# Kernel optimization log

Measured on AMD Instinct MI355X. Metric: run time of the kernel, lower is better.

## Reference

```python
import jax, jax.numpy as jnp
import numpy as np

B, BLOCK_NUM, BLOCK_LEN, DIM = 4, 32, 128, 1024
HEADS = 16
DH = DIM // HEADS  # 64
SEQ_LEN = BLOCK_NUM * BLOCK_LEN  # 4096
LN_EPS = 1e-3  # keras LayerNormalization default epsilon
NEG = -1e10


def setup_inputs() -> dict:
    key = jax.random.key(0)
    ks = jax.random.split(key, 6)
    s = 1.0 / np.sqrt(DIM)
    return {
        "inputs": jax.random.normal(ks[0], (B, BLOCK_NUM, BLOCK_LEN, DIM), jnp.float32),
        "mask": jax.random.randint(ks[1], (B, SEQ_LEN, DIM), 0, 2, jnp.int32),
        "w1": jax.random.normal(ks[2], (DIM, DIM), jnp.float32) * s,
        "b1": jnp.zeros((DIM,), jnp.float32),
        "w2": jax.random.normal(ks[3], (DIM, DIM), jnp.float32) * s,
        "b2": jnp.zeros((DIM,), jnp.float32),
        "w3": jax.random.normal(ks[4], (DIM, DIM), jnp.float32) * s,
        "b3": jnp.zeros((DIM,), jnp.float32),
        "gamma": jnp.ones((DIM,), jnp.float32),
        "beta": jnp.zeros((DIM,), jnp.float32),
    }


def _split_heads(x):
    # [B, bn, bl, DIM] -> [H, B, bn, bl, DH]  (tf.split axis=-1 + concat axis=0)
    return jnp.moveaxis(x.reshape(B, BLOCK_NUM, BLOCK_LEN, HEADS, DH), 3, 0)


def reference(inputs, mask, w1, b1, w2, b2, w3, b3, gamma, beta):
    Q = _split_heads(inputs @ w1 + b1)
    K = _split_heads(inputs @ w2 + b2)
    V = _split_heads(inputs @ w3 + b3)

    # block-local attention scores: [H, B, bn, bl, bl]
    scores = jnp.einsum("hbnqd,hbnkd->hbnqk", Q, K) / np.sqrt(DH)

    # mask: [B, seq, DIM] -> [B, bn, bl, DIM] -> heads -> [H, B, bn, bl, DH]
    m = jnp.moveaxis(
        mask.astype(jnp.float32).reshape(B, BLOCK_NUM, BLOCK_LEN, HEADS, DH), 3, 0
    )
    # block_len (128) > DH (64): take first feature, tile across key axis
    m = jnp.broadcast_to(m[..., :1], (HEADS, B, BLOCK_NUM, BLOCK_LEN, BLOCK_LEN))
    scores = scores + (1.0 - m) * NEG

    attn = jax.nn.softmax(scores, axis=-1)
    out = jnp.einsum("hbnqk,hbnkd->hbnqd", attn, V)
    # merge heads: [H, B, bn, bl, DH] -> [B, bn, bl, DIM]
    out = jnp.moveaxis(out, 0, 3).reshape(B, BLOCK_NUM, BLOCK_LEN, DIM)

    res = out + inputs
    mu = res.mean(axis=-1, keepdims=True)
    var = res.var(axis=-1, keepdims=True)
    return gamma * (res - mu) * jax.lax.rsqrt(var + LN_EPS) + beta
```

## Files before the change

kernel.cpp:

```cpp
#include <hip/hip_runtime.h>
#include <hip/hip_bf16.h>
#include <stdint.h>

#define DIM 1024
#define NTOK 16384
#define SEQ 4096
#define BLKLEN 128
#define NHEAD 16
#define DH 64

typedef short bf16x8 __attribute__((ext_vector_type(8)));
typedef float f32x4 __attribute__((ext_vector_type(4)));

static __device__ __forceinline__ unsigned short f2bf(float f) {
  union { float f; uint32_t u; } v; v.f = f;
  return (unsigned short)((v.u + 0x7FFFu + ((v.u >> 16) & 1u)) >> 16);
}
static __device__ __forceinline__ float bf2f(unsigned short h) {
  union { uint32_t u; float f; } v; v.u = ((uint32_t)h) << 16;
  return v.f;
}
static __device__ __forceinline__ uint32_t pk2(float a, float b) {
  __hip_bfloat162 h = __float22bfloat162_rn(make_float2(a, b));
  union { __hip_bfloat162 h; uint32_t u; } c; c.h = h; return c.u;
}
static __device__ __forceinline__ void cvt8(float4 x, float4 y, uint4& hi, uint4& lo) {
  float f[8] = {x.x, x.y, x.z, x.w, y.x, y.y, y.z, y.w};
  uint32_t h[4], l[4];
#pragma unroll
  for (int i = 0; i < 4; ++i) {
    h[i] = pk2(f[2 * i], f[2 * i + 1]);
    union { uint32_t u; float g; } e0, e1;
    e0.u = h[i] << 16;
    e1.u = h[i] & 0xFFFF0000u;
    l[i] = pk2(f[2 * i] - e0.g, f[2 * i + 1] - e1.g);
  }
  hi = make_uint4(h[0], h[1], h[2], h[3]);
  lo = make_uint4(l[0], l[1], l[2], l[3]);
}

__global__ void wsplit_kernel(const float* __restrict__ w1, const float* __restrict__ w2,
                              const float* __restrict__ w3,
                              unsigned short* __restrict__ hi, unsigned short* __restrict__ lo) {
  const float* w = (blockIdx.z == 0) ? w1 : (blockIdx.z == 1) ? w2 : w3;
  unsigned short* hp = hi + (size_t)blockIdx.z * DIM * DIM;
  unsigned short* lp = lo + (size_t)blockIdx.z * DIM * DIM;
  __shared__ float t[64][65];
  int m0 = blockIdx.x * 64, k0 = blockIdx.y * 64;
  int tx = threadIdx.x, ty = threadIdx.y;
  for (int i = ty; i < 64; i += 4)
    t[i][tx] = w[(size_t)(k0 + i) * DIM + m0 + tx];
  __syncthreads();
  for (int i = ty; i < 64; i += 4) {
    float x = t[tx][i];
    unsigned short h = f2bf(x);
    size_t o = (size_t)(m0 + i) * DIM + k0 + tx;
    hp[o] = h;
    lp[o] = f2bf(x - bf2f(h));
  }
}

#define BK 32
#define AST 40

__global__ __launch_bounds__(256, 2) void qkv_gemm_kernel(
    const float* __restrict__ X,
    const unsigned short* __restrict__ Whi, const unsigned short* __restrict__ Wlo,
    const float* __restrict__ b1, const float* __restrict__ b2, const float* __restrict__ b3,
    float* __restrict__ Qp, float* __restrict__ Kp, float* __restrict__ Vp) {
  __shared__ unsigned short Ah[128 * AST], Al[128 * AST], Bh[128 * AST], Bl[128 * AST];

  int tile_n = blockIdx.x;
  int tile_m = blockIdx.y;
  int wsel = tile_n >> 3;
  int colw0 = (tile_n & 7) * 128;
  const unsigned short* wh = Whi + (size_t)wsel * DIM * DIM;
  const unsigned short* wl = Wlo + (size_t)wsel * DIM * DIM;
  const float* bias = (wsel == 0) ? b1 : (wsel == 1) ? b2 : b3;
  float* o = (wsel == 0) ? Qp : (wsel == 1) ? Kp : Vp;

  int t = threadIdx.x;
  int wid = t >> 6, lane = t & 63;
  int wr = wid >> 1, wc = wid & 1;

  f32x4 acc[4][4];
#pragma unroll
  for (int i = 0; i < 4; ++i)
#pragma unroll
    for (int j = 0; j < 4; ++j) acc[i][j] = (f32x4){0.f, 0.f, 0.f, 0.f};

  int srow = t >> 2;
  int kc = (t & 3) * 8;
  const size_t arow = (size_t)tile_m * 128;

  const float* pa0 = X + (arow + srow) * DIM + kc;
  const float* pa1 = X + (arow + srow + 64) * DIM + kc;
  const unsigned short* pb0 = wh + (size_t)(colw0 + srow) * DIM + kc;
  const unsigned short* pb1 = wh + (size_t)(colw0 + srow + 64) * DIM + kc;
  const unsigned short* plb0 = wl + (size_t)(colw0 + srow) * DIM + kc;
  const unsigned short* plb1 = wl + (size_t)(colw0 + srow + 64) * DIM + kc;

  uint32_t lw0 = srow * AST + kc;
  uint32_t lw1 = (srow + 64) * AST + kc;

  int frow = lane & 15;
  int fk = (lane >> 4) * 8;

  float4 ra00 = *(const float4*)(pa0), ra01 = *(const float4*)(pa0 + 4);
  float4 ra10 = *(const float4*)(pa1), ra11 = *(const float4*)(pa1 + 4);
  uint4 rbh0 = *(const uint4*)(pb0), rbh1 = *(const uint4*)(pb1);
  uint4 rbl0 = *(const uint4*)(plb0), rbl1 = *(const uint4*)(plb1);

  for (int k0 = 0; k0 < DIM; k0 += BK) {
    uint4 ah0, al0, ah1, al1;
    cvt8(ra00, ra01, ah0, al0);
    cvt8(ra10, ra11, ah1, al1);
    __syncthreads();
    *(uint4*)&Ah[lw0] = ah0; *(uint4*)&Ah[lw1] = ah1;
    *(uint4*)&Al[lw0] = al0; *(uint4*)&Al[lw1] = al1;
    *(uint4*)&Bh[lw0] = rbh0; *(uint4*)&Bh[lw1] = rbh1;
    *(uint4*)&Bl[lw0] = rbl0; *(uint4*)&Bl[lw1] = rbl1;
    __syncthreads();
    if (k0 + BK < DIM) {
      int off = k0 + BK;
      ra00 = *(const float4*)(pa0 + off); ra01 = *(const float4*)(pa0 + off + 4);
      ra10 = *(const float4*)(pa1 + off); ra11 = *(const float4*)(pa1 + off + 4);
      rbh0 = *(const uint4*)(pb0 + off); rbh1 = *(const uint4*)(pb1 + off);
      rbl0 = *(const uint4*)(plb0 + off); rbl1 = *(const uint4*)(plb1 + off);
    }
    bf16x8 fah[4], fal[4], fbh[4], fbl[4];
#pragma unroll
    for (int m = 0; m < 4; ++m) {
      int r = wr * 64 + m * 16 + frow;
      fah[m] = *(const bf16x8*)&Ah[r * AST + fk];
      fal[m] = *(const bf16x8*)&Al[r * AST + fk];
    }
#pragma unroll
    for (int n = 0; n < 4; ++n) {
      int c = wc * 64 + n * 16 + frow;
      fbh[n] = *(const bf16x8*)&Bh[c * AST + fk];
      fbl[n] = *(const bf16x8*)&Bl[c * AST + fk];
    }
#pragma unroll
    for (int m = 0; m < 4; ++m)
#pragma unroll
      for (int n = 0; n < 4; ++n) {
        acc[m][n] = __builtin_amdgcn_mfma_f32_16x16x32_bf16(fah[m], fbh[n], acc[m][n], 0, 0, 0);
        acc[m][n] = __builtin_amdgcn_mfma_f32_16x16x32_bf16(fah[m], fbl[n], acc[m][n], 0, 0, 0);
        acc[m][n] = __builtin_amdgcn_mfma_f32_16x16x32_bf16(fal[m], fbh[n], acc[m][n], 0, 0, 0);
      }
  }

  int fgrp = lane >> 4;
#pragma unroll
  for (int n = 0; n < 4; ++n) {
    int col = colw0 + wc * 64 + n * 16 + frow;
    float bv = bias[col];
#pragma unroll
    for (int m = 0; m < 4; ++m) {
      size_t row = arow + wr * 64 + m * 16 + fgrp * 4;
#pragma unroll
      for (int r = 0; r < 4; ++r)
        o[(row + r) * DIM + col] = acc[m][n][r] + bv;
    }
  }
}

__global__ __launch_bounds__(256) void attn_kernel(
    const float* __restrict__ Qg, const float* __restrict__ Kg, const float* Vg,
    const int* __restrict__ mask, const float* __restrict__ inputs, float* out) {
  __shared__ float smem[128 * 132 + 128 * 68];
  float* Qt = smem;
  float* Kt = smem + 64 * 132;
  float* Pt = smem;
  float* Vs = smem + 128 * 132;

  int blk = blockIdx.x;
  int n = blk & 31;
  int b = (blk >> 5) & 3;
  int h = blk >> 7;
  size_t tok0 = (size_t)b * SEQ + (size_t)n * BLKLEN;
  int col0 = h * DH;

  int t = threadIdx.x;
  {
    int r = t >> 1;
    int d0 = (t & 1) * 32;
    const float* qp = Qg + (tok0 + r) * DIM + col0 + d0;
    const float* kp = Kg + (tok0 + r) * DIM + col0 + d0;
    const float* vp = Vg + (tok0 + r) * DIM + col0 + d0;
#pragma unroll
    for (int i = 0; i < 8; ++i) {
      float4 q4 = *(const float4*)(qp + i * 4);
      float4 k4 = *(const float4*)(kp + i * 4);
      float4 v4 = *(const float4*)(vp + i * 4);
      int d = d0 + i * 4;
      Qt[(d + 0) * 132 + r] = q4.x; Qt[(d + 1) * 132 + r] = q4.y;
      Qt[(d + 2) * 132 + r] = q4.z; Qt[(d + 3) * 132 + r] = q4.w;
      Kt[(d + 0) * 132 + r] = k4.x; Kt[(d + 1) * 132 + r] = k4.y;
      Kt[(d + 2) * 132 + r] = k4.z; Kt[(d + 3) * 132 + r] = k4.w;
      *(float4*)&Vs[r * 68 + d] = v4;
    }
  }
  __syncthreads();

  int qt = t >> 4, kt = t & 15;
  int q0 = qt * 8, k0 = kt * 8;
  float s[8][8];
#pragma unroll
  for (int i = 0; i < 8; ++i)
#pragma unroll
    for (int j = 0; j < 8; ++j) s[i][j] = 0.f;

#pragma unroll 4
  for (int d = 0; d < 64; ++d) {
    float4 qa = *(const float4*)&Qt[d * 132 + q0];
    float4 qb = *(const float4*)&Qt[d * 132 + q0 + 4];
    float4 ka = *(const float4*)&Kt[d * 132 + k0];
    float4 kb = *(const float4*)&Kt[d * 132 + k0 + 4];
    float qv[8] = {qa.x, qa.y, qa.z, qa.w, qb.x, qb.y, qb.z, qb.w};
    float kv[8] = {ka.x, ka.y, ka.z, ka.w, kb.x, kb.y, kb.z, kb.w};
#pragma unroll
    for (int i = 0; i < 8; ++i)
#pragma unroll
      for (int j = 0; j < 8; ++j) s[i][j] += qv[i] * kv[j];
  }

  float pen[8];
#pragma unroll
  for (int i = 0; i < 8; ++i)
    pen[i] = (1.0f - (float)mask[(tok0 + q0 + i) * DIM + col0]) * -1e10f;

  float mx[8], sm[8], inv[8];
#pragma unroll
  for (int i = 0; i < 8; ++i) {
    float m0 = -3.4e38f;
#pragma unroll
    for (int j = 0; j < 8; ++j) {
      s[i][j] = s[i][j] * 0.125f + pen[i];
      m0 = fmaxf(m0, s[i][j]);
    }
    mx[i] = m0;
  }
#pragma unroll
  for (int x = 1; x < 16; x <<= 1)
#pragma unroll
    for (int i = 0; i < 8; ++i) mx[i] = fmaxf(mx[i], __shfl_xor(mx[i], x));
#pragma unroll
  for (int i = 0; i < 8; ++i) {
    float a = 0.f;
#pragma unroll
    for (int j = 0; j < 8; ++j) {
      s[i][j] = __expf(s[i][j] - mx[i]);
      a += s[i][j];
    }
    sm[i] = a;
  }
#pragma unroll
  for (int x = 1; x < 16; x <<= 1)
#pragma unroll
    for (int i = 0; i < 8; ++i) sm[i] += __shfl_xor(sm[i], x);
#pragma unroll
  for (int i = 0; i < 8; ++i) inv[i] = 1.0f / sm[i];

  __syncthreads();
#pragma unroll
  for (int j = 0; j < 8; ++j)
#pragma unroll
    for (int i = 0; i < 8; ++i)
      Pt[(k0 + j) * 132 + (q0 + i)] = s[i][j] * inv[i];
  __syncthreads();

  int dt = t & 15;
  int q0b = (t >> 4) * 8;
  int dv0 = dt * 4;
  float o0[8], o1[8], o2[8], o3[8];
#pragma unroll
  for (int i = 0; i < 8; ++i) { o0[i] = 0.f; o1[i] = 0.f; o2[i] = 0.f; o3[i] = 0.f; }

#pragma unroll 4
  for (int k = 0; k < 128; ++k) {
    float4 pa = *(const float4*)&Pt[k * 132 + q0b];
    float4 pb = *(const float4*)&Pt[k * 132 + q0b + 4];
    float4 vv = *(const float4*)&Vs[k * 68 + dv0];
    float pv[8] = {pa.x, pa.y, pa.z, pa.w, pb.x, pb.y, pb.z, pb.w};
#pragma unroll
    for (int i = 0; i < 8; ++i) {
      o0[i] += pv[i] * vv.x;
      o1[i] += pv[i] * vv.y;
      o2[i] += pv[i] * vv.z;
      o3[i] += pv[i] * vv.w;
    }
  }
#pragma unroll
  for (int i = 0; i < 8; ++i) {
    size_t idx = (tok0 + q0b + i) * DIM + col0 + dv0;
    float4 inp = *(const float4*)(inputs + idx);
    float4 r;
    r.x = o0[i] + inp.x; r.y = o1[i] + inp.y; r.z = o2[i] + inp.z; r.w = o3[i] + inp.w;
    *(float4*)(out + idx) = r;
  }
}

__global__ __launch_bounds__(256) void ln_kernel(float* __restrict__ io,
                                                 const float* __restrict__ gamma,
                                                 const float* __restrict__ beta) {
  int row = blockIdx.x;
  int t = threadIdx.x;
  float4 x = *(const float4*)(io + (size_t)row * DIM + t * 4);
  float s = x.x + x.y + x.z + x.w;
  float q = x.x * x.x + x.y * x.y + x.z * x.z + x.w * x.w;
#pragma unroll
  for (int off = 1; off < 64; off <<= 1) {
    s += __shfl_xor(s, off);
    q += __shfl_xor(q, off);
  }
  __shared__ float red[8];
  int wid = t >> 6, lane = t & 63;
  if (lane == 0) { red[wid] = s; red[wid + 4] = q; }
  __syncthreads();
  s = red[0] + red[1] + red[2] + red[3];
  q = red[4] + red[5] + red[6] + red[7];
  float mu = s * (1.0f / 1024.0f);
  float var = q * (1.0f / 1024.0f) - mu * mu;
  float rs = 1.0f / sqrtf(var + 1e-3f);
  float4 g = *(const float4*)(gamma + t * 4);
  float4 be = *(const float4*)(beta + t * 4);
  float4 r;
  r.x = g.x * (x.x - mu) * rs + be.x;
  r.y = g.y * (x.y - mu) * rs + be.y;
  r.z = g.z * (x.z - mu) * rs + be.z;
  r.w = g.w * (x.w - mu) * rs + be.w;
  *(float4*)(io + (size_t)row * DIM + t * 4) = r;
}

extern "C" void kernel_launch(void* const* d_in, const int* in_sizes, int n_in,
                              void* d_out, int out_size, void* d_ws, size_t ws_size,
                              hipStream_t stream) {
  (void)in_sizes; (void)n_in; (void)out_size; (void)ws_size;
  const float* inputs = (const float*)d_in[0];
  const int* mask = (const int*)d_in[1];
  const float* w1 = (const float*)d_in[2];
  const float* b1 = (const float*)d_in[3];
  const float* w2 = (const float*)d_in[4];
  const float* b2 = (const float*)d_in[5];
  const float* w3 = (const float*)d_in[6];
  const float* b3 = (const float*)d_in[7];
  const float* gamma = (const float*)d_in[8];
  const float* beta = (const float*)d_in[9];
  float* out = (float*)d_out;

  char* ws = (char*)d_ws;
  unsigned short* Whi = (unsigned short*)(ws);
  unsigned short* Wlo = (unsigned short*)(ws + ((size_t)6 << 20));
  float* Q = (float*)(ws + ((size_t)12 << 20));
  float* K = (float*)(ws + ((size_t)76 << 20));
  float* V = out;

  hipLaunchKernelGGL(wsplit_kernel, dim3(16, 16, 3), dim3(64, 4), 0, stream,
                     w1, w2, w3, Whi, Wlo);
  hipLaunchKernelGGL(qkv_gemm_kernel, dim3(24, 128), dim3(256), 0, stream,
                     inputs, Whi, Wlo, b1, b2, b3, Q, K, V);
  hipLaunchKernelGGL(attn_kernel, dim3(2048), dim3(256), 0, stream,
                     Q, K, V, mask, inputs, out);
  hipLaunchKernelGGL(ln_kernel, dim3(NTOK), dim3(256), 0, stream,
                     out, gamma, beta);
}
```

Measured before the change: 658.6 us.

## Drop activation low-part in QKV GEMM and store attention Q/K/P as bf16

The QKV GEMM stops splitting the input activations into hi/lo bf16 parts, which removes one of three MFMAs per tile and the Al shared buffer, and raises the occupancy hint to 4. The attention kernel now stores Q, K and the probability matrix in shared memory as bf16 instead of fp32, which halves LDS traffic and footprint and allows two blocks per CU. Both changes lower numerical precision and could push the output past the accuracy tolerance.

```diff
diff --git a/kernel.cpp b/kernel.cpp
--- a/kernel.cpp
+++ b/kernel.cpp
@@ -24,19 +24,13 @@
   __hip_bfloat162 h = __float22bfloat162_rn(make_float2(a, b));
   union { __hip_bfloat162 h; uint32_t u; } c; c.h = h; return c.u;
 }
-static __device__ __forceinline__ void cvt8(float4 x, float4 y, uint4& hi, uint4& lo) {
-  float f[8] = {x.x, x.y, x.z, x.w, y.x, y.y, y.z, y.w};
-  uint32_t h[4], l[4];
-#pragma unroll
-  for (int i = 0; i < 4; ++i) {
-    h[i] = pk2(f[2 * i], f[2 * i + 1]);
-    union { uint32_t u; float g; } e0, e1;
-    e0.u = h[i] << 16;
-    e1.u = h[i] & 0xFFFF0000u;
-    l[i] = pk2(f[2 * i] - e0.g, f[2 * i + 1] - e1.g);
-  }
-  hi = make_uint4(h[0], h[1], h[2], h[3]);
-  lo = make_uint4(l[0], l[1], l[2], l[3]);
+static __device__ __forceinline__ void up2(uint32_t w, float& a, float& b) {
+  union { uint32_t u; float f; } x, y;
+  x.u = w << 16; y.u = w & 0xFFFF0000u;
+  a = x.f; b = y.f;
+}
+static __device__ __forceinline__ uint4 cvt4(float4 x, float4 y) {
+  return make_uint4(pk2(x.x, x.y), pk2(x.z, x.w), pk2(y.x, y.y), pk2(y.z, y.w));
 }
 
 __global__ void wsplit_kernel(const float* __restrict__ w1, const float* __restrict__ w2,
@@ -63,12 +57,12 @@
 #define BK 32
 #define AST 40
 
-__global__ __launch_bounds__(256, 2) void qkv_gemm_kernel(
+__global__ __launch_bounds__(256, 4) void qkv_gemm_kernel(
     const float* __restrict__ X,
     const unsigned short* __restrict__ Whi, const unsigned short* __restrict__ Wlo,
     const float* __restrict__ b1, const float* __restrict__ b2, const float* __restrict__ b3,
     float* __restrict__ Qp, float* __restrict__ Kp, float* __restrict__ Vp) {
-  __shared__ unsigned short Ah[128 * AST], Al[128 * AST], Bh[128 * AST], Bl[128 * AST];
+  __shared__ unsigned short Ah[128 * AST], Bh[128 * AST], Bl[128 * AST];
 
   int tile_n = blockIdx.x;
   int tile_m = blockIdx.y;
@@ -112,12 +106,10 @@
   uint4 rbl0 = *(const uint4*)(plb0), rbl1 = *(const uint4*)(plb1);
 
   for (int k0 = 0; k0 < DIM; k0 += BK) {
-    uint4 ah0, al0, ah1, al1;
-    cvt8(ra00, ra01, ah0, al0);
-    cvt8(ra10, ra11, ah1, al1);
+    uint4 ah0 = cvt4(ra00, ra01);
+    uint4 ah1 = cvt4(ra10, ra11);
     __syncthreads();
     *(uint4*)&Ah[lw0] = ah0; *(uint4*)&Ah[lw1] = ah1;
-    *(uint4*)&Al[lw0] = al0; *(uint4*)&Al[lw1] = al1;
     *(uint4*)&Bh[lw0] = rbh0; *(uint4*)&Bh[lw1] = rbh1;
     *(uint4*)&Bl[lw0] = rbl0; *(uint4*)&Bl[lw1] = rbl1;
     __syncthreads();
@@ -128,12 +120,11 @@
       rbh0 = *(const uint4*)(pb0 + off); rbh1 = *(const uint4*)(pb1 + off);
       rbl0 = *(const uint4*)(plb0 + off); rbl1 = *(const uint4*)(plb1 + off);
     }
-    bf16x8 fah[4], fal[4], fbh[4], fbl[4];
+    bf16x8 fa[4], fbh[4], fbl[4];
 #pragma unroll
     for (int m = 0; m < 4; ++m) {
       int r = wr * 64 + m * 16 + frow;
-      fah[m] = *(const bf16x8*)&Ah[r * AST + fk];
-      fal[m] = *(const bf16x8*)&Al[r * AST + fk];
+      fa[m] = *(const bf16x8*)&Ah[r * AST + fk];
     }
 #pragma unroll
     for (int n = 0; n < 4; ++n) {
@@ -145,9 +136,8 @@
     for (int m = 0; m < 4; ++m)
 #pragma unroll
       for (int n = 0; n < 4; ++n) {
-        acc[m][n] = __builtin_amdgcn_mfma_f32_16x16x32_bf16(fah[m], fbh[n], acc[m][n], 0, 0, 0);
-        acc[m][n] = __builtin_amdgcn_mfma_f32_16x16x32_bf16(fah[m], fbl[n], acc[m][n], 0, 0, 0);
-        acc[m][n] = __builtin_amdgcn_mfma_f32_16x16x32_bf16(fal[m], fbh[n], acc[m][n], 0, 0, 0);
+        acc[m][n] = __builtin_amdgcn_mfma_f32_16x16x32_bf16(fa[m], fbh[n], acc[m][n], 0, 0, 0);
+        acc[m][n] = __builtin_amdgcn_mfma_f32_16x16x32_bf16(fa[m], fbl[n], acc[m][n], 0, 0, 0);
       }
   }
 
@@ -166,14 +156,16 @@
   }
 }
 
-__global__ __launch_bounds__(256) void attn_kernel(
+#define PST 136
+
+__global__ __launch_bounds__(256, 2) void attn_kernel(
     const float* __restrict__ Qg, const float* __restrict__ Kg, const float* Vg,
     const int* __restrict__ mask, const float* __restrict__ inputs, float* out) {
-  __shared__ float smem[128 * 132 + 128 * 68];
-  float* Qt = smem;
-  float* Kt = smem + 64 * 132;
-  float* Pt = smem;
-  float* Vs = smem + 128 * 132;
+  __shared__ __align__(16) unsigned char smem[69632];
+  unsigned short* Qt = (unsigned short*)smem;
+  unsigned short* Kt = Qt + 64 * PST;
+  unsigned short* Pt = (unsigned short*)smem;
+  float* Vs = (float*)(smem + 2 * 64 * PST * 2);
 
   int blk = blockIdx.x;
   int n = blk & 31;
@@ -195,10 +187,10 @@
       float4 k4 = *(const float4*)(kp + i * 4);
       float4 v4 = *(const float4*)(vp + i * 4);
       int d = d0 + i * 4;
-      Qt[(d + 0) * 132 + r] = q4.x; Qt[(d + 1) * 132 + r] = q4.y;
-      Qt[(d + 2) * 132 + r] = q4.z; Qt[(d + 3) * 132 + r] = q4.w;
-      Kt[(d + 0) * 132 + r] = k4.x; Kt[(d + 1) * 132 + r] = k4.y;
-      Kt[(d + 2) * 132 + r] = k4.z; Kt[(d + 3) * 132 + r] = k4.w;
+      Qt[(d + 0) * PST + r] = f2bf(q4.x); Qt[(d + 1) * PST + r] = f2bf(q4.y);
+      Qt[(d + 2) * PST + r] = f2bf(q4.z); Qt[(d + 3) * PST + r] = f2bf(q4.w);
+      Kt[(d + 0) * PST + r] = f2bf(k4.x); Kt[(d + 1) * PST + r] = f2bf(k4.y);
+      Kt[(d + 2) * PST + r] = f2bf(k4.z); Kt[(d + 3) * PST + r] = f2bf(k4.w);
       *(float4*)&Vs[r * 68 + d] = v4;
     }
   }
@@ -214,12 +206,13 @@
 
 #pragma unroll 4
   for (int d = 0; d < 64; ++d) {
-    float4 qa = *(const float4*)&Qt[d * 132 + q0];
-    float4 qb = *(const float4*)&Qt[d * 132 + q0 + 4];
-    float4 ka = *(const float4*)&Kt[d * 132 + k0];
-    float4 kb = *(const float4*)&Kt[d * 132 + k0 + 4];
-    float qv[8] = {qa.x, qa.y, qa.z, qa.w, qb.x, qb.y, qb.z, qb.w};
-    float kv[8] = {ka.x, ka.y, ka.z, ka.w, kb.x, kb.y, kb.z, kb.w};
+    uint4 qw = *(const uint4*)&Qt[d * PST + q0];
+    uint4 kw = *(const uint4*)&Kt[d * PST + k0];
+    float qv[8], kv[8];
+    up2(qw.x, qv[0], qv[1]); up2(qw.y, qv[2], qv[3]);
+    up2(qw.z, qv[4], qv[5]); up2(qw.w, qv[6], qv[7]);
+    up2(kw.x, kv[0], kv[1]); up2(kw.y, kv[2], kv[3]);
+    up2(kw.z, kv[4], kv[5]); up2(kw.w, kv[6], kv[7]);
 #pragma unroll
     for (int i = 0; i < 8; ++i)
 #pragma unroll
@@ -267,8 +260,10 @@
 #pragma unroll
   for (int j = 0; j < 8; ++j)
 #pragma unroll
-    for (int i = 0; i < 8; ++i)
-      Pt[(k0 + j) * 132 + (q0 + i)] = s[i][j] * inv[i];
+    for (int i = 0; i < 8; i += 2) {
+      uint32_t pw = pk2(s[i][j] * inv[i], s[i + 1][j] * inv[i + 1]);
+      *(uint32_t*)&Pt[(k0 + j) * PST + q0 + i] = pw;
+    }
   __syncthreads();
 
   int dt = t & 15;
@@ -280,10 +275,11 @@
 
 #pragma unroll 4
   for (int k = 0; k < 128; ++k) {
-    float4 pa = *(const float4*)&Pt[k * 132 + q0b];
-    float4 pb = *(const float4*)&Pt[k * 132 + q0b + 4];
+    uint4 pw = *(const uint4*)&Pt[k * PST + q0b];
+    float pv[8];
+    up2(pw.x, pv[0], pv[1]); up2(pw.y, pv[2], pv[3]);
+    up2(pw.z, pv[4], pv[5]); up2(pw.w, pv[6], pv[7]);
     float4 vv = *(const float4*)&Vs[k * 68 + dv0];
-    float pv[8] = {pa.x, pa.y, pa.z, pa.w, pb.x, pb.y, pb.z, pb.w};
 #pragma unroll
     for (int i = 0; i < 8; ++i) {
       o0[i] += pv[i] * vv.x;
```

Measured after the change: 1.293 ms. 1.96x slower.
